# Kernel optimization log

Measured on AMD Instinct MI355X. Metric: run time of the kernel, lower is better.

Reference implementation:

```python
import jax, jax.numpy as jnp
import numpy as np
from jax import lax

# Model dims (match init_kwargs / input_specs)
E = 32      # n_routed_experts
H = 1024    # hidden_size
I = 768     # moe_intermediate_size
T = 4096    # num_tokens
K = 4       # top_k
CAP = 1024  # per-expert capacity; mean load = T*K/E = 512, std ~22 -> no overflow


def setup_inputs() -> dict:
    key = jax.random.key(0)
    k1, k2, k3, k4, k5 = jax.random.split(key, 5)
    hidden_states = jax.random.normal(k1, (T, H), jnp.float32)
    top_k_index = jax.random.randint(k2, (T, K), 0, E, dtype=jnp.int32)
    top_k_weights = jax.random.uniform(k3, (T, K), jnp.float32)
    gate_up_proj = jax.random.normal(k4, (E, 2 * I, H), jnp.float32) * 0.02
    down_proj = jax.random.normal(k5, (E, H, I), jnp.float32) * 0.02
    return {
        "hidden_states": hidden_states,
        "top_k_index": top_k_index,
        "top_k_weights": top_k_weights,
        "gate_up_proj": gate_up_proj,
        "down_proj": down_proj,
    }


def moe_forward(hidden_states, top_k_weights, gate_up_proj, down_proj, top_k_index):
    """Token-sorted grouped SwiGLU MoE, identical math to the per-expert torch loop."""
    num_tokens, hidden = hidden_states.shape
    top_k = top_k_index.shape[1]
    n_assign = num_tokens * top_k

    flat_e = top_k_index.reshape(-1)                       # [N] expert id per assignment
    flat_w = top_k_weights.reshape(-1)                     # [N]
    tok_of = jnp.arange(n_assign, dtype=jnp.int32) // top_k  # [N] source token

    # Sort assignments by expert id so each expert's tokens are contiguous.
    order = jnp.argsort(flat_e)
    s_e = flat_e[order]
    s_tok = tok_of[order]
    s_w = flat_w[order]

    counts = jnp.zeros((E,), jnp.int32).at[flat_e].add(1)          # tokens per expert
    offsets = jnp.concatenate([jnp.zeros((1,), jnp.int32),
                               jnp.cumsum(counts)[:-1].astype(jnp.int32)])

    xs = hidden_states[s_tok]                                       # [N, H] gathered inputs
    # Pad by CAP rows so fixed-size dynamic slices never clamp.
    xs_pad = jnp.concatenate([xs, jnp.zeros((CAP, hidden), xs.dtype)], axis=0)
    s_tok_pad = jnp.concatenate([s_tok, jnp.zeros((CAP,), jnp.int32)])
    s_w_pad = jnp.concatenate([s_w, jnp.zeros((CAP,), s_w.dtype)])

    def per_expert(e):
        off = offsets[e]
        chunk = lax.dynamic_slice(xs_pad, (off, 0), (CAP, hidden))   # [CAP, H]
        gu = chunk @ gate_up_proj[e].T                               # [CAP, 2I]
        gate, up = jnp.split(gu, 2, axis=-1)
        h = jax.nn.silu(gate) * up                                   # SwiGLU
        out = h @ down_proj[e].T                                     # [CAP, H]
        pos = off + jnp.arange(CAP, dtype=jnp.int32)
        valid = jnp.arange(CAP) < counts[e]
        w = jnp.where(valid, s_w_pad[pos], 0.0)
        dest = jnp.where(valid, s_tok_pad[pos], num_tokens)          # invalid -> dropped row
        return out * w[:, None], dest

    outs, dests = jax.vmap(per_expert)(jnp.arange(E))                # [E, CAP, H], [E, CAP]
    y = jnp.zeros((num_tokens + 1, hidden), hidden_states.dtype)
    y = y.at[dests.reshape(-1)].add(outs.reshape(-1, hidden))
    return y[:num_tokens]


def reference(hidden_states, top_k_index, top_k_weights, gate_up_proj, down_proj):
    return moe_forward(hidden_states, top_k_weights, gate_up_proj, down_proj, top_k_index)
```

## Files before the change

kernel.cpp:

```cpp
#include <hip/hip_runtime.h>
#include <hip/hip_bf16.h>

#define E_ 32
#define H_ 1024
#define I_ 768
#define I2_ 1536
#define T_ 4096
#define K_ 4
#define CAP_ 1024
#define NSLOT_ (E_*CAP_)

typedef __attribute__((ext_vector_type(8))) short short8;
typedef __attribute__((ext_vector_type(4))) float f32x4;

__device__ __forceinline__ short f2bf(float f) {
    __hip_bfloat16 h = __float2bfloat16(f);
    return __builtin_bit_cast(short, h);
}

typedef __attribute__((address_space(3))) void lds_void;
typedef const __attribute__((address_space(1))) void glob_void;

__device__ __forceinline__ void gload16(const void* g, void* l) {
    __builtin_amdgcn_global_load_lds((glob_void*)g, (lds_void*)l, 16, 0, 0);
}


__global__ void k_init(int* __restrict__ cursor, int* __restrict__ s_tok,
                       float* __restrict__ s_w) {
    int i = blockIdx.x * 256 + threadIdx.x;
    if (i < E_) cursor[i] = 0;
    if (i < NSLOT_) { s_tok[i] = 0; s_w[i] = 0.f; }
}

__global__ void k_cast(const float* __restrict__ in, short* __restrict__ outb) {
    int i = blockIdx.x * 256 + threadIdx.x;
    const float* p = in + (size_t)i * 8;
    f32x4 a = *(const f32x4*)p;
    f32x4 b = *(const f32x4*)(p + 4);
    short8 o;
    o[0]=f2bf(a[0]); o[1]=f2bf(a[1]); o[2]=f2bf(a[2]); o[3]=f2bf(a[3]);
    o[4]=f2bf(b[0]); o[5]=f2bf(b[1]); o[6]=f2bf(b[2]); o[7]=f2bf(b[3]);
    *(short8*)(outb + (size_t)i * 8) = o;
}

__global__ void k_scatter(const int* __restrict__ tki, const float* __restrict__ tkw,
                          int* __restrict__ cursor, int* __restrict__ s_tok,
                          float* __restrict__ s_w, int* __restrict__ pos) {
    int n = blockIdx.x * 256 + threadIdx.x;
    if (n >= T_ * K_) return;
    int e = tki[n];
    int p = atomicAdd(cursor + e, 1);
    if (p < CAP_) {
        s_tok[e * CAP_ + p] = n >> 2;
        s_w[e * CAP_ + p]   = tkw[n];
        pos[n] = e * CAP_ + p;
    } else {
        pos[n] = -1;
    }
}

__global__ __launch_bounds__(256) void k_gemm1(
    const short* __restrict__ Xb, const float* __restrict__ W1,
    const int* __restrict__ s_tok, const int* __restrict__ counts,
    short* __restrict__ Hb)
{
    __shared__ alignas(16) short As[128 * 64];
    __shared__ alignas(16) short Bs[128 * 64];

    int bid = blockIdx.x;
    bid = (bid & 7) * (3072 / 8) + (bid >> 3);

    int e   = bid / 96;
    int rem = bid % 96;
    int mt = rem / 12, nt = rem % 12;
    int cnt = min(counts[e], CAP_);
    int row0 = mt * 128;
    if (row0 >= cnt) return;
    int gc0 = nt * 64;

    int tid = threadIdx.x, wid = tid >> 6, lane = tid & 63;
    int wm = wid >> 1, wn = wid & 1;

    unsigned offA[4];
#pragma unroll
    for (int j = 0; j < 4; ++j) {
        int cl = j * 256 + tid;
        int row = cl >> 3, cpos = cl & 7;
        int tok = s_tok[e * CAP_ + row0 + row];
        offA[j] = (unsigned)tok * H_ + ((cpos ^ (row & 7)) * 8);
    }
    const float* w1e = W1 + (size_t)e * I2_ * H_;
    unsigned gB[4]; unsigned ldsB[4];
#pragma unroll
    for (int j = 0; j < 4; ++j) {
        int cl = j * 256 + tid;
        int row = cl >> 3, cpos = cl & 7;
        int wr = (row < 64) ? (gc0 + row) : (768 + gc0 + (row - 64));
        gB[j]   = (unsigned)wr * H_ + cpos * 8;
        ldsB[j] = (unsigned)row * 64 + ((cpos ^ (row & 7)) * 8);
    }

    f32x4 accg[4][2], accu[4][2];
#pragma unroll
    for (int m = 0; m < 4; ++m)
#pragma unroll
        for (int n = 0; n < 2; ++n) {
            accg[m][n] = (f32x4){0.f, 0.f, 0.f, 0.f};
            accu[m][n] = (f32x4){0.f, 0.f, 0.f, 0.f};
        }

    for (int kt = 0; kt < H_ / 64; ++kt) {
        int k0 = kt * 64;
        f32x4 b0[4], b1[4];
#pragma unroll
        for (int j = 0; j < 4; ++j) {
            const float* p = w1e + gB[j] + k0;
            b0[j] = *(const f32x4*)p;
            b1[j] = *(const f32x4*)(p + 4);
        }
#pragma unroll
        for (int j = 0; j < 4; ++j)
            gload16(Xb + offA[j] + k0, (char*)As + j * 4096 + wid * 1024);
#pragma unroll
        for (int j = 0; j < 4; ++j) {
            short8 t;
            t[0]=f2bf(b0[j][0]); t[1]=f2bf(b0[j][1]); t[2]=f2bf(b0[j][2]); t[3]=f2bf(b0[j][3]);
            t[4]=f2bf(b1[j][0]); t[5]=f2bf(b1[j][1]); t[6]=f2bf(b1[j][2]); t[7]=f2bf(b1[j][3]);
            *(short8*)&Bs[ldsB[j]] = t;
        }
        __syncthreads();

#pragma unroll
        for (int kk = 0; kk < 2; ++kk) {
            short8 a[4];
#pragma unroll
            for (int m = 0; m < 4; ++m) {
                int r = wm * 64 + m * 16 + (lane & 15);
                int c = (kk * 4 + (lane >> 4)) ^ (r & 7);
                a[m] = *(const short8*)&As[r * 64 + c * 8];
            }
            short8 bg[2], bu[2];
#pragma unroll
            for (int n = 0; n < 2; ++n) {
                int brg = wn * 32 + n * 16 + (lane & 15);
                int cg = (kk * 4 + (lane >> 4)) ^ (brg & 7);
                bg[n] = *(const short8*)&Bs[brg * 64 + cg * 8];
                int bru = 64 + wn * 32 + n * 16 + (lane & 15);
                int cu = (kk * 4 + (lane >> 4)) ^ (bru & 7);
                bu[n] = *(const short8*)&Bs[bru * 64 + cu * 8];
            }
#pragma unroll
            for (int m = 0; m < 4; ++m)
#pragma unroll
                for (int n = 0; n < 2; ++n) {
                    accg[m][n] = __builtin_amdgcn_mfma_f32_16x16x32_bf16(a[m], bg[n], accg[m][n], 0, 0, 0);
                    accu[m][n] = __builtin_amdgcn_mfma_f32_16x16x32_bf16(a[m], bu[n], accu[m][n], 0, 0, 0);
                }
        }
        __syncthreads();
    }

#pragma unroll
    for (int m = 0; m < 4; ++m) {
        int rb = row0 + wm * 64 + m * 16 + ((lane >> 4) * 4);
#pragma unroll
        for (int n = 0; n < 2; ++n) {
            int col = gc0 + wn * 32 + n * 16 + (lane & 15);
#pragma unroll
            for (int q = 0; q < 4; ++q) {
                float g = accg[m][n][q], u = accu[m][n][q];
                float h = (g / (1.f + __expf(-g))) * u;
                Hb[(size_t)(e * CAP_ + rb + q) * I_ + col] = f2bf(h);
            }
        }
    }
}

__global__ __launch_bounds__(256) void k_gemm2(
    const short* __restrict__ Hb, const float* __restrict__ W2,
    const float* __restrict__ s_w, const int* __restrict__ counts,
    float* __restrict__ Oslot)
{
    __shared__ alignas(16) short Ah[128 * 64];
    __shared__ alignas(16) short Bs[128 * 64];

    int bid = blockIdx.x;
    bid = (bid & 7) * (2048 / 8) + (bid >> 3);

    int e = bid / 64;
    int rem = bid % 64;
    int mt = rem / 8, nt = rem % 8;
    int cnt = min(counts[e], CAP_);
    int row0 = mt * 128;
    if (row0 >= cnt) return;
    int nc0 = nt * 128;

    int tid = threadIdx.x, wid = tid >> 6, lane = tid & 63;
    int wm = wid >> 1, wn = wid & 1;

    unsigned offA[4];
#pragma unroll
    for (int j = 0; j < 4; ++j) {
        int cl = j * 256 + tid;
        int row = cl >> 3, cpos = cl & 7;
        offA[j] = (unsigned)(e * CAP_ + row0 + row) * I_ + ((cpos ^ (row & 7)) * 8);
    }
    const float* w2e = W2 + (size_t)e * H_ * I_;
    unsigned gB[4]; unsigned ldsB[4];
#pragma unroll
    for (int j = 0; j < 4; ++j) {
        int cl = j * 256 + tid;
        int row = cl >> 3, cpos = cl & 7;
        gB[j]   = (unsigned)(nc0 + row) * I_ + cpos * 8;
        ldsB[j] = (unsigned)row * 64 + ((cpos ^ (row & 7)) * 8);
    }

    f32x4 acc[4][4];
#pragma unroll
    for (int m = 0; m < 4; ++m)
#pragma unroll
        for (int n = 0; n < 4; ++n) acc[m][n] = (f32x4){0.f, 0.f, 0.f, 0.f};

    for (int kt = 0; kt < I_ / 64; ++kt) {
        int k0 = kt * 64;
        f32x4 b0[4], b1[4];
#pragma unroll
        for (int j = 0; j < 4; ++j) {
            const float* p = w2e + gB[j] + k0;
            b0[j] = *(const f32x4*)p;
            b1[j] = *(const f32x4*)(p + 4);
        }
#pragma unroll
        for (int j = 0; j < 4; ++j)
            gload16(Hb + offA[j] + k0, (char*)Ah + j * 4096 + wid * 1024);
#pragma unroll
        for (int j = 0; j < 4; ++j) {
            short8 t;
            t[0]=f2bf(b0[j][0]); t[1]=f2bf(b0[j][1]); t[2]=f2bf(b0[j][2]); t[3]=f2bf(b0[j][3]);
            t[4]=f2bf(b1[j][0]); t[5]=f2bf(b1[j][1]); t[6]=f2bf(b1[j][2]); t[7]=f2bf(b1[j][3]);
            *(short8*)&Bs[ldsB[j]] = t;
        }
        __syncthreads();

#pragma unroll
        for (int kk = 0; kk < 2; ++kk) {
            short8 a[4];
#pragma unroll
            for (int m = 0; m < 4; ++m) {
                int r = wm * 64 + m * 16 + (lane & 15);
                int c = (kk * 4 + (lane >> 4)) ^ (r & 7);
                a[m] = *(const short8*)&Ah[r * 64 + c * 8];
            }
            short8 b[4];
#pragma unroll
            for (int n = 0; n < 4; ++n) {
                int br = wn * 64 + n * 16 + (lane & 15);
                int c = (kk * 4 + (lane >> 4)) ^ (br & 7);
                b[n] = *(const short8*)&Bs[br * 64 + c * 8];
            }
#pragma unroll
            for (int m = 0; m < 4; ++m)
#pragma unroll
                for (int n = 0; n < 4; ++n)
                    acc[m][n] = __builtin_amdgcn_mfma_f32_16x16x32_bf16(a[m], b[n], acc[m][n], 0, 0, 0);
        }
        __syncthreads();
    }

#pragma unroll
    for (int m = 0; m < 4; ++m) {
#pragma unroll
        for (int q = 0; q < 4; ++q) {
            int i = row0 + wm * 64 + m * 16 + ((lane >> 4) * 4) + q;
            if (i < cnt) {
                float w = s_w[e * CAP_ + i];
                float* orow = Oslot + (size_t)(e * CAP_ + i) * H_;
#pragma unroll
                for (int n = 0; n < 4; ++n)
                    orow[nc0 + wn * 64 + n * 16 + (lane & 15)] = acc[m][n][q] * w;
            }
        }
    }
}

__global__ __launch_bounds__(256) void k_gather(
    const float* __restrict__ Oslot, const int* __restrict__ pos,
    float* __restrict__ out)
{
    int t = blockIdx.x;
    int c = threadIdx.x * 4;
    int p0 = pos[t * 4 + 0], p1 = pos[t * 4 + 1];
    int p2 = pos[t * 4 + 2], p3 = pos[t * 4 + 3];
    f32x4 s = (f32x4){0.f, 0.f, 0.f, 0.f};
    if (p0 >= 0) { f32x4 v = *(const f32x4*)&Oslot[(size_t)p0 * H_ + c]; s += v; }
    if (p1 >= 0) { f32x4 v = *(const f32x4*)&Oslot[(size_t)p1 * H_ + c]; s += v; }
    if (p2 >= 0) { f32x4 v = *(const f32x4*)&Oslot[(size_t)p2 * H_ + c]; s += v; }
    if (p3 >= 0) { f32x4 v = *(const f32x4*)&Oslot[(size_t)p3 * H_ + c]; s += v; }
    *(f32x4*)&out[(size_t)t * H_ + c] = s;
}


extern "C" void kernel_launch(void* const* d_in, const int* in_sizes, int n_in,
                              void* d_out, int out_size, void* d_ws, size_t ws_size,
                              hipStream_t stream) {
    const float* hs  = (const float*)d_in[0];
    const int*   tki = (const int*)d_in[1];
    const float* tkw = (const float*)d_in[2];
    const float* w1  = (const float*)d_in[3];
    const float* w2  = (const float*)d_in[4];
    float* out = (float*)d_out;

    char* ws = (char*)d_ws;
    int*   cursor = (int*)ws;
    int*   s_tok  = (int*)(ws + 4096);
    float* s_w    = (float*)(ws + 4096 + NSLOT_ * 4);
    int*   pos    = (int*)(ws + 4096 + NSLOT_ * 8);
    char*  big0   = ws + 4096 + NSLOT_ * 8 + (size_t)T_ * K_ * 4;
    short* Xb     = (short*)big0;
    short* Hb     = (short*)(big0 + (size_t)T_ * H_ * 2);
    float* Oslot  = (float*)(big0 + (size_t)T_ * H_ * 2 + (size_t)NSLOT_ * I_ * 2);

    hipLaunchKernelGGL(k_init, dim3(NSLOT_ / 256), dim3(256), 0, stream, cursor, s_tok, s_w);
    hipLaunchKernelGGL(k_cast, dim3((T_ * H_) / 2048), dim3(256), 0, stream, hs, Xb);
    hipLaunchKernelGGL(k_scatter, dim3((T_ * K_) / 256), dim3(256), 0, stream, tki, tkw, cursor, s_tok, s_w, pos);
    hipLaunchKernelGGL(k_gemm1, dim3(E_ * 8 * 12), dim3(256), 0, stream, Xb, w1, s_tok, cursor, Hb);
    hipLaunchKernelGGL(k_gemm2, dim3(E_ * 8 * 8), dim3(256), 0, stream, Hb, w2, s_w, cursor, Oslot);
    hipLaunchKernelGGL(k_gather, dim3(T_), dim3(256), 0, stream, Oslot, pos, out);
}
```

Before: 238.8 us.

## Double-buffer LDS tiles in both expert GEMMs to overlap loads with MFMA

Both grouped GEMM kernels now keep two LDS buffers for the A and B tiles. The next K-slice is prefetched, with fp32 weights held in registers and activations sent via global_load_lds, while MFMAs run on the current slice. The converted weights are written to the other buffer after compute, so each iteration needs one barrier instead of two. The cost is twice the LDS (64KB per block) and more live registers, which may lower occupancy.

Measured after the change: 264.0 us. 10.6% more time.

```diff
diff --git a/kernel.cpp b/kernel.cpp
--- a/kernel.cpp
+++ b/kernel.cpp
@@ -25,6 +25,13 @@
     __builtin_amdgcn_global_load_lds((glob_void*)g, (lds_void*)l, 16, 0, 0);
 }
 
+__device__ __forceinline__ short8 cvt8(f32x4 x, f32x4 y) {
+    short8 t;
+    t[0]=f2bf(x[0]); t[1]=f2bf(x[1]); t[2]=f2bf(x[2]); t[3]=f2bf(x[3]);
+    t[4]=f2bf(y[0]); t[5]=f2bf(y[1]); t[6]=f2bf(y[2]); t[7]=f2bf(y[3]);
+    return t;
+}
+
 
 __global__ void k_init(int* __restrict__ cursor, int* __restrict__ s_tok,
                        float* __restrict__ s_w) {
@@ -38,10 +45,7 @@
     const float* p = in + (size_t)i * 8;
     f32x4 a = *(const f32x4*)p;
     f32x4 b = *(const f32x4*)(p + 4);
-    short8 o;
-    o[0]=f2bf(a[0]); o[1]=f2bf(a[1]); o[2]=f2bf(a[2]); o[3]=f2bf(a[3]);
-    o[4]=f2bf(b[0]); o[5]=f2bf(b[1]); o[6]=f2bf(b[2]); o[7]=f2bf(b[3]);
-    *(short8*)(outb + (size_t)i * 8) = o;
+    *(short8*)(outb + (size_t)i * 8) = cvt8(a, b);
 }
 
 __global__ void k_scatter(const int* __restrict__ tki, const float* __restrict__ tkw,
@@ -65,8 +69,8 @@
     const int* __restrict__ s_tok, const int* __restrict__ counts,
     short* __restrict__ Hb)
 {
-    __shared__ alignas(16) short As[128 * 64];
-    __shared__ alignas(16) short Bs[128 * 64];
+    __shared__ alignas(16) short As[2][128 * 64];
+    __shared__ alignas(16) short Bs[2][128 * 64];
 
     int bid = blockIdx.x;
     bid = (bid & 7) * (3072 / 8) + (bid >> 3);
@@ -110,27 +114,37 @@
             accu[m][n] = (f32x4){0.f, 0.f, 0.f, 0.f};
         }
 
-    for (int kt = 0; kt < H_ / 64; ++kt) {
-        int k0 = kt * 64;
-        f32x4 b0[4], b1[4];
-#pragma unroll
-        for (int j = 0; j < 4; ++j) {
-            const float* p = w1e + gB[j] + k0;
-            b0[j] = *(const f32x4*)p;
-            b1[j] = *(const f32x4*)(p + 4);
-        }
-#pragma unroll
-        for (int j = 0; j < 4; ++j)
-            gload16(Xb + offA[j] + k0, (char*)As + j * 4096 + wid * 1024);
-#pragma unroll
-        for (int j = 0; j < 4; ++j) {
-            short8 t;
-            t[0]=f2bf(b0[j][0]); t[1]=f2bf(b0[j][1]); t[2]=f2bf(b0[j][2]); t[3]=f2bf(b0[j][3]);
-            t[4]=f2bf(b1[j][0]); t[5]=f2bf(b1[j][1]); t[6]=f2bf(b1[j][2]); t[7]=f2bf(b1[j][3]);
-            *(short8*)&Bs[ldsB[j]] = t;
-        }
-        __syncthreads();
-
+    f32x4 nb0[4], nb1[4];
+#pragma unroll
+    for (int j = 0; j < 4; ++j) {
+        const float* p = w1e + gB[j];
+        nb0[j] = *(const f32x4*)p; nb1[j] = *(const f32x4*)(p + 4);
+    }
+#pragma unroll
+    for (int j = 0; j < 4; ++j)
+        gload16(Xb + offA[j], (char*)As[0] + j * 4096 + wid * 1024);
+#pragma unroll
+    for (int j = 0; j < 4; ++j)
+        *(short8*)&Bs[0][ldsB[j]] = cvt8(nb0[j], nb1[j]);
+    __syncthreads();
+
+    const int NT = H_ / 64;
+    for (int kt = 0; kt < NT; ++kt) {
+        int cur = kt & 1, nxt = cur ^ 1;
+        bool pf = (kt + 1) < NT;
+        if (pf) {
+            int k0n = (kt + 1) * 64;
+#pragma unroll
+            for (int j = 0; j < 4; ++j) {
+                const float* p = w1e + gB[j] + k0n;
+                nb0[j] = *(const f32x4*)p; nb1[j] = *(const f32x4*)(p + 4);
+            }
+#pragma unroll
+            for (int j = 0; j < 4; ++j)
+                gload16(Xb + offA[j] + k0n, (char*)As[nxt] + j * 4096 + wid * 1024);
+        }
+        const short* Asc = As[cur];
+        const short* Bsc = Bs[cur];
 #pragma unroll
         for (int kk = 0; kk < 2; ++kk) {
             short8 a[4];
@@ -138,17 +152,17 @@
             for (int m = 0; m < 4; ++m) {
                 int r = wm * 64 + m * 16 + (lane & 15);
                 int c = (kk * 4 + (lane >> 4)) ^ (r & 7);
-                a[m] = *(const short8*)&As[r * 64 + c * 8];
+                a[m] = *(const short8*)&Asc[r * 64 + c * 8];
             }
             short8 bg[2], bu[2];
 #pragma unroll
             for (int n = 0; n < 2; ++n) {
                 int brg = wn * 32 + n * 16 + (lane & 15);
                 int cg = (kk * 4 + (lane >> 4)) ^ (brg & 7);
-                bg[n] = *(const short8*)&Bs[brg * 64 + cg * 8];
+                bg[n] = *(const short8*)&Bsc[brg * 64 + cg * 8];
                 int bru = 64 + wn * 32 + n * 16 + (lane & 15);
                 int cu = (kk * 4 + (lane >> 4)) ^ (bru & 7);
-                bu[n] = *(const short8*)&Bs[bru * 64 + cu * 8];
+                bu[n] = *(const short8*)&Bsc[bru * 64 + cu * 8];
             }
 #pragma unroll
             for (int m = 0; m < 4; ++m)
@@ -157,6 +171,11 @@
                     accg[m][n] = __builtin_amdgcn_mfma_f32_16x16x32_bf16(a[m], bg[n], accg[m][n], 0, 0, 0);
                     accu[m][n] = __builtin_amdgcn_mfma_f32_16x16x32_bf16(a[m], bu[n], accu[m][n], 0, 0, 0);
                 }
+        }
+        if (pf) {
+#pragma unroll
+            for (int j = 0; j < 4; ++j)
+                *(short8*)&Bs[nxt][ldsB[j]] = cvt8(nb0[j], nb1[j]);
         }
         __syncthreads();
     }
@@ -182,8 +201,8 @@
     const float* __restrict__ s_w, const int* __restrict__ counts,
     float* __restrict__ Oslot)
 {
-    __shared__ alignas(16) short Ah[128 * 64];
-    __shared__ alignas(16) short Bs[128 * 64];
+    __shared__ alignas(16) short Ah[2][128 * 64];
+    __shared__ alignas(16) short Bs[2][128 * 64];
 
     int bid = blockIdx.x;
     bid = (bid & 7) * (2048 / 8) + (bid >> 3);
@@ -222,27 +241,37 @@
 #pragma unroll
         for (int n = 0; n < 4; ++n) acc[m][n] = (f32x4){0.f, 0.f, 0.f, 0.f};
 
-    for (int kt = 0; kt < I_ / 64; ++kt) {
-        int k0 = kt * 64;
-        f32x4 b0[4], b1[4];
-#pragma unroll
-        for (int j = 0; j < 4; ++j) {
-            const float* p = w2e + gB[j] + k0;
-            b0[j] = *(const f32x4*)p;
-            b1[j] = *(const f32x4*)(p + 4);
-        }
-#pragma unroll
-        for (int j = 0; j < 4; ++j)
-            gload16(Hb + offA[j] + k0, (char*)Ah + j * 4096 + wid * 1024);
-#pragma unroll
-        for (int j = 0; j < 4; ++j) {
-            short8 t;
-            t[0]=f2bf(b0[j][0]); t[1]=f2bf(b0[j][1]); t[2]=f2bf(b0[j][2]); t[3]=f2bf(b0[j][3]);
-            t[4]=f2bf(b1[j][0]); t[5]=f2bf(b1[j][1]); t[6]=f2bf(b1[j][2]); t[7]=f2bf(b1[j][3]);
-            *(short8*)&Bs[ldsB[j]] = t;
-        }
-        __syncthreads();
-
+    f32x4 nb0[4], nb1[4];
+#pragma unroll
+    for (int j = 0; j < 4; ++j) {
+        const float* p = w2e + gB[j];
+        nb0[j] = *(const f32x4*)p; nb1[j] = *(const f32x4*)(p + 4);
+    }
+#pragma unroll
+    for (int j = 0; j < 4; ++j)
+        gload16(Hb + offA[j], (char*)Ah[0] + j * 4096 + wid * 1024);
+#pragma unroll
+    for (int j = 0; j < 4; ++j)
+        *(short8*)&Bs[0][ldsB[j]] = cvt8(nb0[j], nb1[j]);
+    __syncthreads();
+
+    const int NT = I_ / 64;
+    for (int kt = 0; kt < NT; ++kt) {
+        int cur = kt & 1, nxt = cur ^ 1;
+        bool pf = (kt + 1) < NT;
+        if (pf) {
+            int k0n = (kt + 1) * 64;
+#pragma unroll
+            for (int j = 0; j < 4; ++j) {
+                const float* p = w2e + gB[j] + k0n;
+                nb0[j] = *(const f32x4*)p; nb1[j] = *(const f32x4*)(p + 4);
+            }
+#pragma unroll
+            for (int j = 0; j < 4; ++j)
+                gload16(Hb + offA[j] + k0n, (char*)Ah[nxt] + j * 4096 + wid * 1024);
+        }
+        const short* Asc = Ah[cur];
+        const short* Bsc = Bs[cur];
 #pragma unroll
         for (int kk = 0; kk < 2; ++kk) {
             short8 a[4];
@@ -250,20 +279,25 @@
             for (int m = 0; m < 4; ++m) {
                 int r = wm * 64 + m * 16 + (lane & 15);
                 int c = (kk * 4 + (lane >> 4)) ^ (r & 7);
-                a[m] = *(const short8*)&Ah[r * 64 + c * 8];
+                a[m] = *(const short8*)&Asc[r * 64 + c * 8];
             }
             short8 b[4];
 #pragma unroll
             for (int n = 0; n < 4; ++n) {
                 int br = wn * 64 + n * 16 + (lane & 15);
                 int c = (kk * 4 + (lane >> 4)) ^ (br & 7);
-                b[n] = *(const short8*)&Bs[br * 64 + c * 8];
+                b[n] = *(const short8*)&Bsc[br * 64 + c * 8];
             }
 #pragma unroll
             for (int m = 0; m < 4; ++m)
 #pragma unroll
                 for (int n = 0; n < 4; ++n)
                     acc[m][n] = __builtin_amdgcn_mfma_f32_16x16x32_bf16(a[m], b[n], acc[m][n], 0, 0, 0);
+        }
+        if (pf) {
+#pragma unroll
+            for (int j = 0; j < 4; ++j)
+                *(short8*)&Bs[nxt][ldsB[j]] = cvt8(nb0[j], nb1[j]);
         }
         __syncthreads();
     }
```

## Software-pipeline both expert GEMMs with double-buffered A tiles and register-prefetched weights

Applied to the files above, without the earlier changes.

Both grouped GEMM kernels now prefetch the next K-tile while computing the current one. The activation tile is loaded asynchronously into a second LDS buffer, and the fp32 weights are held in a second register set before conversion to bf16. Hand-written s_waitcnt/s_barrier sequences replace __syncthreads so that only the previous tile's loads must complete before compute starts. Launch bounds also request 3 blocks per SM. The cost is extra LDS and registers, and the correctness of the pipeline depends on the manual vmcnt counting.

Result: slower. 274.9 us (+15.1%).

```diff
diff --git a/kernel.cpp b/kernel.cpp
--- a/kernel.cpp
+++ b/kernel.cpp
@@ -25,6 +25,13 @@
     __builtin_amdgcn_global_load_lds((glob_void*)g, (lds_void*)l, 16, 0, 0);
 }
 
+__device__ __forceinline__ short8 cvt8(f32x4 x, f32x4 y) {
+    short8 t;
+    t[0]=f2bf(x[0]); t[1]=f2bf(x[1]); t[2]=f2bf(x[2]); t[3]=f2bf(x[3]);
+    t[4]=f2bf(y[0]); t[5]=f2bf(y[1]); t[6]=f2bf(y[2]); t[7]=f2bf(y[3]);
+    return t;
+}
+
 
 __global__ void k_init(int* __restrict__ cursor, int* __restrict__ s_tok,
                        float* __restrict__ s_w) {
@@ -38,10 +45,7 @@
     const float* p = in + (size_t)i * 8;
     f32x4 a = *(const f32x4*)p;
     f32x4 b = *(const f32x4*)(p + 4);
-    short8 o;
-    o[0]=f2bf(a[0]); o[1]=f2bf(a[1]); o[2]=f2bf(a[2]); o[3]=f2bf(a[3]);
-    o[4]=f2bf(b[0]); o[5]=f2bf(b[1]); o[6]=f2bf(b[2]); o[7]=f2bf(b[3]);
-    *(short8*)(outb + (size_t)i * 8) = o;
+    *(short8*)(outb + (size_t)i * 8) = cvt8(a, b);
 }
 
 __global__ void k_scatter(const int* __restrict__ tki, const float* __restrict__ tkw,
@@ -60,12 +64,61 @@
     }
 }
 
-__global__ __launch_bounds__(256) void k_gemm1(
+
+#define G1_COMPUTE(ASRC) \
+  _Pragma("unroll") \
+  for (int kk = 0; kk < 2; ++kk) { \
+      short8 a[4]; \
+      _Pragma("unroll") \
+      for (int m = 0; m < 4; ++m) { \
+          int r = wm * 64 + m * 16 + (lane & 15); \
+          int c = (kk * 4 + (lane >> 4)) ^ (r & 7); \
+          a[m] = *(const short8*)&(ASRC)[r * 64 + c * 8]; \
+      } \
+      short8 bg[2], bu[2]; \
+      _Pragma("unroll") \
+      for (int n = 0; n < 2; ++n) { \
+          int brg = wn * 32 + n * 16 + (lane & 15); \
+          int cg = (kk * 4 + (lane >> 4)) ^ (brg & 7); \
+          bg[n] = *(const short8*)&Bs[brg * 64 + cg * 8]; \
+          int bru = 64 + wn * 32 + n * 16 + (lane & 15); \
+          int cu = (kk * 4 + (lane >> 4)) ^ (bru & 7); \
+          bu[n] = *(const short8*)&Bs[bru * 64 + cu * 8]; \
+      } \
+      _Pragma("unroll") \
+      for (int m = 0; m < 4; ++m) \
+          _Pragma("unroll") \
+          for (int n = 0; n < 2; ++n) { \
+              accg[m][n] = __builtin_amdgcn_mfma_f32_16x16x32_bf16(a[m], bg[n], accg[m][n], 0, 0, 0); \
+              accu[m][n] = __builtin_amdgcn_mfma_f32_16x16x32_bf16(a[m], bu[n], accu[m][n], 0, 0, 0); \
+          } \
+  }
+
+#define G1_STEP(KT, CUR, NXT, C0, C1, L0, L1) \
+  _Pragma("unroll") \
+  for (int j = 0; j < 4; ++j) \
+      *(short8*)&Bs[ldsB[j]] = cvt8(C0[j], C1[j]); \
+  { \
+      int knext = ((KT) + 1 < 16) ? ((KT) + 1) * 64 : 0; \
+      _Pragma("unroll") \
+      for (int j = 0; j < 4; ++j) { \
+          const float* p = w1e + gB[j] + knext; \
+          L0[j] = *(const f32x4*)p; L1[j] = *(const f32x4*)(p + 4); \
+      } \
+      _Pragma("unroll") \
+      for (int j = 0; j < 4; ++j) \
+          gload16(Xb + offA[j] + knext, (char*)(NXT) + j * 4096 + wid * 1024); \
+  } \
+  asm volatile("s_waitcnt vmcnt(12) lgkmcnt(0)\n\ts_barrier" ::: "memory"); \
+  G1_COMPUTE(CUR) \
+  asm volatile("s_barrier" ::: "memory");
+
+__global__ __launch_bounds__(256, 3) void k_gemm1(
     const short* __restrict__ Xb, const float* __restrict__ W1,
     const int* __restrict__ s_tok, const int* __restrict__ counts,
     short* __restrict__ Hb)
 {
-    __shared__ alignas(16) short As[128 * 64];
+    __shared__ alignas(16) short AsBuf[2][128 * 64];
     __shared__ alignas(16) short Bs[128 * 64];
 
     int bid = blockIdx.x;
@@ -110,56 +163,24 @@
             accu[m][n] = (f32x4){0.f, 0.f, 0.f, 0.f};
         }
 
-    for (int kt = 0; kt < H_ / 64; ++kt) {
-        int k0 = kt * 64;
-        f32x4 b0[4], b1[4];
-#pragma unroll
-        for (int j = 0; j < 4; ++j) {
-            const float* p = w1e + gB[j] + k0;
-            b0[j] = *(const f32x4*)p;
-            b1[j] = *(const f32x4*)(p + 4);
-        }
-#pragma unroll
-        for (int j = 0; j < 4; ++j)
-            gload16(Xb + offA[j] + k0, (char*)As + j * 4096 + wid * 1024);
-#pragma unroll
-        for (int j = 0; j < 4; ++j) {
-            short8 t;
-            t[0]=f2bf(b0[j][0]); t[1]=f2bf(b0[j][1]); t[2]=f2bf(b0[j][2]); t[3]=f2bf(b0[j][3]);
-            t[4]=f2bf(b1[j][0]); t[5]=f2bf(b1[j][1]); t[6]=f2bf(b1[j][2]); t[7]=f2bf(b1[j][3]);
-            *(short8*)&Bs[ldsB[j]] = t;
-        }
-        __syncthreads();
-
-#pragma unroll
-        for (int kk = 0; kk < 2; ++kk) {
-            short8 a[4];
-#pragma unroll
-            for (int m = 0; m < 4; ++m) {
-                int r = wm * 64 + m * 16 + (lane & 15);
-                int c = (kk * 4 + (lane >> 4)) ^ (r & 7);
-                a[m] = *(const short8*)&As[r * 64 + c * 8];
-            }
-            short8 bg[2], bu[2];
-#pragma unroll
-            for (int n = 0; n < 2; ++n) {
-                int brg = wn * 32 + n * 16 + (lane & 15);
-                int cg = (kk * 4 + (lane >> 4)) ^ (brg & 7);
-                bg[n] = *(const short8*)&Bs[brg * 64 + cg * 8];
-                int bru = 64 + wn * 32 + n * 16 + (lane & 15);
-                int cu = (kk * 4 + (lane >> 4)) ^ (bru & 7);
-                bu[n] = *(const short8*)&Bs[bru * 64 + cu * 8];
-            }
-#pragma unroll
-            for (int m = 0; m < 4; ++m)
-#pragma unroll
-                for (int n = 0; n < 2; ++n) {
-                    accg[m][n] = __builtin_amdgcn_mfma_f32_16x16x32_bf16(a[m], bg[n], accg[m][n], 0, 0, 0);
-                    accu[m][n] = __builtin_amdgcn_mfma_f32_16x16x32_bf16(a[m], bu[n], accu[m][n], 0, 0, 0);
-                }
-        }
-        __syncthreads();
-    }
+    short* As0 = AsBuf[0];
+    short* As1 = AsBuf[1];
+    f32x4 b0a[4], b1a[4], b0b[4], b1b[4];
+
+#pragma unroll
+    for (int j = 0; j < 4; ++j) {
+        const float* p = w1e + gB[j];
+        b0a[j] = *(const f32x4*)p; b1a[j] = *(const f32x4*)(p + 4);
+    }
+#pragma unroll
+    for (int j = 0; j < 4; ++j)
+        gload16(Xb + offA[j], (char*)As0 + j * 4096 + wid * 1024);
+
+    for (int kt = 0; kt < 16; kt += 2) {
+        G1_STEP(kt,     As0, As1, b0a, b1a, b0b, b1b)
+        G1_STEP(kt + 1, As1, As0, b0b, b1b, b0a, b1a)
+    }
+    asm volatile("s_waitcnt vmcnt(0)" ::: "memory");
 
 #pragma unroll
     for (int m = 0; m < 4; ++m) {
@@ -177,12 +198,56 @@
     }
 }
 
-__global__ __launch_bounds__(256) void k_gemm2(
+
+#define G2_COMPUTE(ASRC) \
+  _Pragma("unroll") \
+  for (int kk = 0; kk < 2; ++kk) { \
+      short8 a[4]; \
+      _Pragma("unroll") \
+      for (int m = 0; m < 4; ++m) { \
+          int r = wm * 64 + m * 16 + (lane & 15); \
+          int c = (kk * 4 + (lane >> 4)) ^ (r & 7); \
+          a[m] = *(const short8*)&(ASRC)[r * 64 + c * 8]; \
+      } \
+      short8 b[4]; \
+      _Pragma("unroll") \
+      for (int n = 0; n < 4; ++n) { \
+          int br = wn * 64 + n * 16 + (lane & 15); \
+          int c = (kk * 4 + (lane >> 4)) ^ (br & 7); \
+          b[n] = *(const short8*)&Bs[br * 64 + c * 8]; \
+      } \
+      _Pragma("unroll") \
+      for (int m = 0; m < 4; ++m) \
+          _Pragma("unroll") \
+          for (int n = 0; n < 4; ++n) \
+              acc[m][n] = __builtin_amdgcn_mfma_f32_16x16x32_bf16(a[m], b[n], acc[m][n], 0, 0, 0); \
+  }
+
+#define G2_STEP(KT, CUR, NXT, C0, C1, L0, L1) \
+  _Pragma("unroll") \
+  for (int j = 0; j < 4; ++j) \
+      *(short8*)&Bs[ldsB[j]] = cvt8(C0[j], C1[j]); \
+  { \
+      int knext = ((KT) + 1 < 12) ? ((KT) + 1) * 64 : 0; \
+      _Pragma("unroll") \
+      for (int j = 0; j < 4; ++j) { \
+          const float* p = w2e + gB[j] + knext; \
+          L0[j] = *(const f32x4*)p; L1[j] = *(const f32x4*)(p + 4); \
+      } \
+      _Pragma("unroll") \
+      for (int j = 0; j < 4; ++j) \
+          gload16(Hb + offA[j] + knext, (char*)(NXT) + j * 4096 + wid * 1024); \
+  } \
+  asm volatile("s_waitcnt vmcnt(12) lgkmcnt(0)\n\ts_barrier" ::: "memory"); \
+  G2_COMPUTE(CUR) \
+  asm volatile("s_barrier" ::: "memory");
+
+__global__ __launch_bounds__(256, 3) void k_gemm2(
     const short* __restrict__ Hb, const float* __restrict__ W2,
     const float* __restrict__ s_w, const int* __restrict__ counts,
     float* __restrict__ Oslot)
 {
-    __shared__ alignas(16) short Ah[128 * 64];
+    __shared__ alignas(16) short AhBuf[2][128 * 64];
     __shared__ alignas(16) short Bs[128 * 64];
 
     int bid = blockIdx.x;
@@ -222,51 +287,24 @@
 #pragma unroll
         for (int n = 0; n < 4; ++n) acc[m][n] = (f32x4){0.f, 0.f, 0.f, 0.f};
 
-    for (int kt = 0; kt < I_ / 64; ++kt) {
-        int k0 = kt * 64;
-        f32x4 b0[4], b1[4];
-#pragma unroll
-        for (int j = 0; j < 4; ++j) {
-            const float* p = w2e + gB[j] + k0;
-            b0[j] = *(const f32x4*)p;
-            b1[j] = *(const f32x4*)(p + 4);
-        }
-#pragma unroll
-        for (int j = 0; j < 4; ++j)
-            gload16(Hb + offA[j] + k0, (char*)Ah + j * 4096 + wid * 1024);
-#pragma unroll
-        for (int j = 0; j < 4; ++j) {
-            short8 t;
-            t[0]=f2bf(b0[j][0]); t[1]=f2bf(b0[j][1]); t[2]=f2bf(b0[j][2]); t[3]=f2bf(b0[j][3]);
-            t[4]=f2bf(b1[j][0]); t[5]=f2bf(b1[j][1]); t[6]=f2bf(b1[j][2]); t[7]=f2bf(b1[j][3]);
-            *(short8*)&Bs[ldsB[j]] = t;
-        }
-        __syncthreads();
-
-#pragma unroll
-        for (int kk = 0; kk < 2; ++kk) {
-            short8 a[4];
-#pragma unroll
-            for (int m = 0; m < 4; ++m) {
-                int r = wm * 64 + m * 16 + (lane & 15);
-                int c = (kk * 4 + (lane >> 4)) ^ (r & 7);
-                a[m] = *(const short8*)&Ah[r * 64 + c * 8];
-            }
-            short8 b[4];
-#pragma unroll
-            for (int n = 0; n < 4; ++n) {
-                int br = wn * 64 + n * 16 + (lane & 15);
-                int c = (kk * 4 + (lane >> 4)) ^ (br & 7);
-                b[n] = *(const short8*)&Bs[br * 64 + c * 8];
-            }
-#pragma unroll
-            for (int m = 0; m < 4; ++m)
-#pragma unroll
-                for (int n = 0; n < 4; ++n)
-                    acc[m][n] = __builtin_amdgcn_mfma_f32_16x16x32_bf16(a[m], b[n], acc[m][n], 0, 0, 0);
-        }
-        __syncthreads();
-    }
+    short* Ah0 = AhBuf[0];
+    short* Ah1 = AhBuf[1];
+    f32x4 b0a[4], b1a[4], b0b[4], b1b[4];
+
+#pragma unroll
+    for (int j = 0; j < 4; ++j) {
+        const float* p = w2e + gB[j];
+        b0a[j] = *(const f32x4*)p; b1a[j] = *(const f32x4*)(p + 4);
+    }
+#pragma unroll
+    for (int j = 0; j < 4; ++j)
+        gload16(Hb + offA[j], (char*)Ah0 + j * 4096 + wid * 1024);
+
+    for (int kt = 0; kt < 12; kt += 2) {
+        G2_STEP(kt,     Ah0, Ah1, b0a, b1a, b0b, b1b)
+        G2_STEP(kt + 1, Ah1, Ah0, b0b, b1b, b0a, b1a)
+    }
+    asm volatile("s_waitcnt vmcnt(0)" ::: "memory");
 
 #pragma unroll
     for (int m = 0; m < 4; ++m) {
```
